# Kernel optimization log

Hardware: AMD Instinct MI355X
Metric: run time of the kernel (lower is better)

## Reference

```python
import jax, jax.numpy as jnp
import numpy as np

N_ZONE, E_ZONE = 100000, 2000000
N_OUT, E_OUT = 50000, 1000000
N_GND, E_GND = 50000, 1000000
HID = 64


def _gcn_conv(x, W, b, edge_index, edge_weight, num_nodes):
    """PyG GCNConv with normalize=True, add_self_loops=True (fill_value=1).
    out[i] = sum_{e: col[e]=i} d^-1/2[row]*w_e*d^-1/2[col] * (xW)[row[e]]
             + d^-1[i]*(xW)[i] + b
    """
    row, col = edge_index[0], edge_index[1]
    ew = edge_weight.reshape(-1)  # [E,1] -> [E]
    # degree includes self-loop weight of 1
    deg = jax.ops.segment_sum(ew, col, num_segments=num_nodes) + 1.0
    dinv = jnp.where(deg > 0, jax.lax.rsqrt(deg), 0.0)
    norm = dinv[row] * ew * dinv[col]  # [E]
    h = x @ W  # [N, HID] transform first (tiny in-dim)
    agg = jax.ops.segment_sum(norm[:, None] * h[row], col, num_segments=num_nodes)
    agg = agg + (dinv * dinv)[:, None] * h  # self-loop term
    return agg + b


def setup_inputs() -> dict:
    key = jax.random.key(0)
    ks = jax.random.split(key, 16)
    inp = {}
    inp["x_zone"] = jax.random.normal(ks[0], (N_ZONE, 2), dtype=jnp.float32)
    inp["x_outdoor"] = jax.random.normal(ks[1], (N_OUT, 3), dtype=jnp.float32)
    inp["x_ground"] = jax.random.normal(ks[2], (N_GND, 1), dtype=jnp.float32)
    inp["edge_index_zone"] = jax.random.randint(ks[3], (2, E_ZONE), 0, N_ZONE, dtype=jnp.int32)
    inp["edge_index_outdoor"] = jax.random.randint(ks[4], (2, E_OUT), 0, N_OUT, dtype=jnp.int32)
    inp["edge_index_ground"] = jax.random.randint(ks[5], (2, E_GND), 0, N_GND, dtype=jnp.int32)
    # learned params: GCN weights/biases + per-edge attribute parameters
    inp["W_zone"] = jax.random.normal(ks[6], (2, HID), dtype=jnp.float32) * 0.5
    inp["W_outdoor"] = jax.random.normal(ks[7], (3, HID), dtype=jnp.float32) * 0.5
    inp["W_ground"] = jax.random.normal(ks[8], (1, HID), dtype=jnp.float32) * 0.5
    inp["b_zone"] = jnp.zeros((HID,), dtype=jnp.float32)
    inp["b_outdoor"] = jnp.zeros((HID,), dtype=jnp.float32)
    inp["b_ground"] = jnp.zeros((HID,), dtype=jnp.float32)
    # positive edge weights so symmetric normalization deg^-1/2 is finite
    inp["edge_attr_zone"] = jax.random.uniform(ks[9], (E_ZONE, 1), dtype=jnp.float32, minval=0.1, maxval=1.0)
    inp["edge_attr_outdoor"] = jax.random.uniform(ks[10], (E_OUT, 1), dtype=jnp.float32, minval=0.1, maxval=1.0)
    inp["edge_attr_ground"] = jax.random.uniform(ks[11], (E_GND, 1), dtype=jnp.float32, minval=0.1, maxval=1.0)
    return inp


def reference(x_zone, x_outdoor, x_ground,
              edge_index_zone, edge_index_outdoor, edge_index_ground,
              W_zone, W_outdoor, W_ground,
              b_zone, b_outdoor, b_ground,
              edge_attr_zone, edge_attr_outdoor, edge_attr_ground):
    z = _gcn_conv(x_zone, W_zone, b_zone, edge_index_zone, edge_attr_zone, N_ZONE)
    o = _gcn_conv(x_outdoor, W_outdoor, b_outdoor, edge_index_outdoor, edge_attr_outdoor, N_OUT)
    g = _gcn_conv(x_ground, W_ground, b_ground, edge_index_ground, edge_attr_ground, N_GND)
    return (jax.nn.relu(z), jax.nn.relu(o), jax.nn.relu(g))
```

## Files before the change

kernel.cpp:

```cpp
#include <hip/hip_runtime.h>

#define N_ZONE 100000
#define E_ZONE 2000000
#define N_OUT  50000
#define E_OUT  1000000
#define N_GND  50000
#define E_GND  1000000
#define HID    64
#define N_TOT   (N_ZONE + N_OUT + N_GND)
#define E_TOTAL (E_ZONE + E_OUT + E_GND)

#define RANGE   2048
#define RSHIFT  11
#define NBZ     49
#define NBO     25
#define NBG     25
#define NBUCKET (NBZ + NBO + NBG)
#define SL      16
#define CAP     49152
#define OUT_PAD_BASE (NBZ * RANGE)
#define GND_PAD_BASE ((NBZ + NBO) * RANGE)
#define PAD_TOT      (NBUCKET * RANGE)

#define CHUNK  4096
#define NCHUNK ((E_TOTAL + CHUNK - 1) / CHUNK)

#define KUF 8

#define WCUR  0
#define WREC  128
#define WPDEG (WREC + 2 * NBUCKET * CAP)
#define WPSZ  (WPDEG + NBUCKET * SL * RANGE)
#define WPSO  (WPSZ + NBZ * SL * RANGE * 2)
#define WPSG  (WPSO + NBO * SL * RANGE * 3)
#define WDINV (WPSG + NBG * SL * RANGE)
#define WYZ   (WDINV + PAD_TOT)
#define WYO   (WYZ + 2 * N_ZONE)
#define WYG   (WYO + 4 * N_OUT)
#define WUZ   (WYG + N_GND)
#define WUO   (WUZ + 2 * N_ZONE)
#define WUG   (WUO + 4 * N_OUT)
#define WTOT  (WUG + N_GND)
#define FAST_WS_BYTES ((size_t)WTOT * 4)

__global__ void k_bin(const int* __restrict__ eiz, const float* __restrict__ wz,
                      const int* __restrict__ eio, const float* __restrict__ wo,
                      const int* __restrict__ eig, const float* __restrict__ wg,
                      unsigned* __restrict__ cur, uint2* __restrict__ rec) {
    __shared__ unsigned la[CHUNK];
    __shared__ float    lw[CHUNK];
    __shared__ unsigned char lbk[CHUNK];
    __shared__ unsigned hist[NBUCKET];
    __shared__ unsigned sbase[NBUCKET + 1];
    __shared__ unsigned gbase[NBUCKET];
    int tid = threadIdx.x;
    for (int b = tid; b < NBUCKET; b += 256) hist[b] = 0;
    __syncthreads();
    int t0 = blockIdx.x * CHUNK;
    unsigned mya[CHUNK / 256], mybk[CHUNK / 256], myr[CHUNK / 256];
    float myw[CHUNK / 256];
#pragma unroll
    for (int i = 0; i < CHUNK / 256; i++) {
        int t = t0 + i * 256 + tid;
        unsigned b = 0xFFFFFFFFu;
        if (t < E_TOTAL) {
            int row, col; float w;
            if (t < E_ZONE) { row = eiz[t]; col = eiz[E_ZONE + t]; w = wz[t]; b = col >> RSHIFT; }
            else if (t < E_ZONE + E_OUT) { int e = t - E_ZONE; row = eio[e]; col = eio[E_OUT + e]; w = wo[e]; b = NBZ + (col >> RSHIFT); }
            else { int e = t - E_ZONE - E_OUT; row = eig[e]; col = eig[E_GND + e]; w = wg[e]; b = NBZ + NBO + (col >> RSHIFT); }
            mya[i] = ((unsigned)(col & (RANGE - 1)) << 17) | (unsigned)row;
            myw[i] = w;
            myr[i] = atomicAdd(&hist[b], 1u);
        }
        mybk[i] = b;
    }
    __syncthreads();
    if (tid == 0) {
        unsigned acc = 0;
        for (int b = 0; b < NBUCKET; b++) { sbase[b] = acc; acc += hist[b]; }
        sbase[NBUCKET] = acc;
    }
    __syncthreads();
    if (tid < NBUCKET)
        gbase[tid] = hist[tid] ? atomicAdd(&cur[tid], hist[tid]) : 0u;
#pragma unroll
    for (int i = 0; i < CHUNK / 256; i++) {
        if (mybk[i] < NBUCKET) {
            unsigned p = sbase[mybk[i]] + myr[i];
            la[p] = mya[i]; lw[p] = myw[i];
            lbk[p] = (unsigned char)mybk[i];
        }
    }
    __syncthreads();
    unsigned total = sbase[NBUCKET];
    unsigned p = tid;
    for (; p + 768u < total; p += 1024u) {
#pragma unroll
        for (int u = 0; u < 4; u++) {
            unsigned pp = p + 256u * u;
            unsigned b = lbk[pp];
            unsigned idx = b * CAP + gbase[b] + (pp - sbase[b]);
            rec[idx] = make_uint2(la[pp], __float_as_uint(lw[pp]));
        }
    }
    for (; p < total; p += 256u) {
        unsigned b = lbk[p];
        unsigned idx = b * CAP + gbase[b] + (p - sbase[b]);
        rec[idx] = make_uint2(la[p], __float_as_uint(lw[p]));
    }
}

__global__ void k_degp(const uint2* __restrict__ rec, const unsigned* __restrict__ cur,
                       float* __restrict__ pdeg) {
    __shared__ float deg[RANGE];
    int r = blockIdx.x / SL, sl = blockIdx.x % SL, tid = threadIdx.x;
    for (int i = tid; i < RANGE; i += 256) deg[i] = 0.0f;
    __syncthreads();
    unsigned c = cur[r];
    size_t b0 = (size_t)r * CAP;
    unsigned per = (c + SL - 1) / SL;
    unsigned s0 = sl * per, s1 = s0 + per; if (s1 > c) s1 = c;
    unsigned j = s0 + tid;
    for (; j + 256u * (KUF - 1) < s1; j += 256u * KUF) {
        uint2 q[KUF];
#pragma unroll
        for (int u = 0; u < KUF; u++) q[u] = rec[b0 + j + 256u * u];
#pragma unroll
        for (int u = 0; u < KUF; u++)
            atomicAdd(&deg[(q[u].x >> 17) & (RANGE - 1)], __uint_as_float(q[u].y));
    }
    if (j < s1) {
        uint2 q[KUF];
#pragma unroll
        for (int u = 0; u < KUF; u++) {
            unsigned jj = j + 256u * u;
            q[u] = rec[b0 + (jj < s1 ? jj : j)];
        }
#pragma unroll
        for (int u = 0; u < KUF; u++)
            if (j + 256u * u < s1)
                atomicAdd(&deg[(q[u].x >> 17) & (RANGE - 1)], __uint_as_float(q[u].y));
    }
    __syncthreads();
    float* o = pdeg + (size_t)blockIdx.x * RANGE;
    for (int i = tid * 4; i < RANGE; i += 1024)
        *(float4*)&o[i] = *(float4*)&deg[i];
}

__global__ void k_dinvy(const float* __restrict__ xz, const float* __restrict__ xo,
                        const float* __restrict__ xg, float* __restrict__ ws) {
    int p = blockIdx.x * blockDim.x + threadIdx.x;
    if (p >= PAD_TOT) return;
    int r = p >> RSHIFT, i = p & (RANGE - 1);
    float d = 1.0f;
#pragma unroll
    for (int sl = 0; sl < SL; sl++)
        d += ws[WPDEG + (size_t)(r * SL + sl) * RANGE + i];
    float di = rsqrtf(d);
    ws[WDINV + p] = di;
    if (p < OUT_PAD_BASE) {
        if (p < N_ZONE) {
            ws[WYZ + 2 * p]     = di * xz[2 * p];
            ws[WYZ + 2 * p + 1] = di * xz[2 * p + 1];
        }
    } else if (p < GND_PAD_BASE) {
        int idx = p - OUT_PAD_BASE;
        if (idx < N_OUT) {
            ws[WYO + 4 * idx]     = di * xo[3 * idx];
            ws[WYO + 4 * idx + 1] = di * xo[3 * idx + 1];
            ws[WYO + 4 * idx + 2] = di * xo[3 * idx + 2];
            ws[WYO + 4 * idx + 3] = 0.0f;
        }
    } else {
        int idx = p - GND_PAD_BASE;
        if (idx < N_GND) ws[WYG + idx] = di * xg[idx];
    }
}

__global__ void k_sp(float* __restrict__ ws) {
    __shared__ __align__(16) float s[RANGE * 3];
    int r = blockIdx.x / SL, sl = blockIdx.x % SL, tid = threadIdx.x;
    const unsigned* cur = (const unsigned*)(ws + WCUR);
    const uint2* rec = (const uint2*)(ws + WREC);
    int ch, rg; size_t yoff, psoff;
    if (r < NBZ)            { ch = 2; rg = r;             yoff = WYZ; psoff = WPSZ; }
    else if (r < NBZ + NBO) { ch = 3; rg = r - NBZ;       yoff = WYO; psoff = WPSO; }
    else                    { ch = 1; rg = r - NBZ - NBO; yoff = WYG; psoff = WPSG; }
    int tot = RANGE * ch;
    for (int i = tid; i < tot; i += 256) s[i] = 0.0f;
    __syncthreads();
    unsigned c = cur[r];
    size_t b0 = (size_t)r * CAP;
    unsigned per = (c + SL - 1) / SL;
    unsigned s0 = sl * per, s1 = s0 + per; if (s1 > c) s1 = c;
    if (ch == 2) {
        const float2* y = (const float2*)(ws + yoff);
        unsigned j = s0 + tid;
        for (; j + 256u * (KUF - 1) < s1; j += 256u * KUF) {
            uint2 q[KUF];
#pragma unroll
            for (int u = 0; u < KUF; u++) q[u] = rec[b0 + j + 256u * u];
            float2 yv[KUF];
#pragma unroll
            for (int u = 0; u < KUF; u++) yv[u] = y[q[u].x & 0x1FFFFu];
#pragma unroll
            for (int u = 0; u < KUF; u++) {
                unsigned colr = (q[u].x >> 17) & (RANGE - 1);
                float w = __uint_as_float(q[u].y);
                atomicAdd(&s[colr * 2],     w * yv[u].x);
                atomicAdd(&s[colr * 2 + 1], w * yv[u].y);
            }
        }
        if (j < s1) {
            uint2 q[KUF];
#pragma unroll
            for (int u = 0; u < KUF; u++) {
                unsigned jj = j + 256u * u;
                q[u] = rec[b0 + (jj < s1 ? jj : j)];
            }
            float2 yv[KUF];
#pragma unroll
            for (int u = 0; u < KUF; u++) yv[u] = y[q[u].x & 0x1FFFFu];
#pragma unroll
            for (int u = 0; u < KUF; u++)
                if (j + 256u * u < s1) {
                    unsigned colr = (q[u].x >> 17) & (RANGE - 1);
                    float w = __uint_as_float(q[u].y);
                    atomicAdd(&s[colr * 2],     w * yv[u].x);
                    atomicAdd(&s[colr * 2 + 1], w * yv[u].y);
                }
        }
    } else if (ch == 3) {
        const float4* y = (const float4*)(ws + yoff);
        unsigned j = s0 + tid;
        for (; j + 256u * (KUF - 1) < s1; j += 256u * KUF) {
            uint2 q[KUF];
#pragma unroll
            for (int u = 0; u < KUF; u++) q[u] = rec[b0 + j + 256u * u];
            float4 yv[KUF];
#pragma unroll
            for (int u = 0; u < KUF; u++) yv[u] = y[q[u].x & 0x1FFFFu];
#pragma unroll
            for (int u = 0; u < KUF; u++) {
                unsigned colr = (q[u].x >> 17) & (RANGE - 1);
                float w = __uint_as_float(q[u].y);
                atomicAdd(&s[colr * 3],     w * yv[u].x);
                atomicAdd(&s[colr * 3 + 1], w * yv[u].y);
                atomicAdd(&s[colr * 3 + 2], w * yv[u].z);
            }
        }
        if (j < s1) {
            uint2 q[KUF];
#pragma unroll
            for (int u = 0; u < KUF; u++) {
                unsigned jj = j + 256u * u;
                q[u] = rec[b0 + (jj < s1 ? jj : j)];
            }
            float4 yv[KUF];
#pragma unroll
            for (int u = 0; u < KUF; u++) yv[u] = y[q[u].x & 0x1FFFFu];
#pragma unroll
            for (int u = 0; u < KUF; u++)
                if (j + 256u * u < s1) {
                    unsigned colr = (q[u].x >> 17) & (RANGE - 1);
                    float w = __uint_as_float(q[u].y);
                    atomicAdd(&s[colr * 3],     w * yv[u].x);
                    atomicAdd(&s[colr * 3 + 1], w * yv[u].y);
                    atomicAdd(&s[colr * 3 + 2], w * yv[u].z);
                }
        }
    } else {
        const float* y = ws + yoff;
        unsigned j = s0 + tid;
        for (; j + 256u * (KUF - 1) < s1; j += 256u * KUF) {
            uint2 q[KUF];
#pragma unroll
            for (int u = 0; u < KUF; u++) q[u] = rec[b0 + j + 256u * u];
            float yv[KUF];
#pragma unroll
            for (int u = 0; u < KUF; u++) yv[u] = y[q[u].x & 0x1FFFFu];
#pragma unroll
            for (int u = 0; u < KUF; u++)
                atomicAdd(&s[(q[u].x >> 17) & (RANGE - 1)], __uint_as_float(q[u].y) * yv[u]);
        }
        if (j < s1) {
            uint2 q[KUF];
#pragma unroll
            for (int u = 0; u < KUF; u++) {
                unsigned jj = j + 256u * u;
                q[u] = rec[b0 + (jj < s1 ? jj : j)];
            }
            float yv[KUF];
#pragma unroll
            for (int u = 0; u < KUF; u++) yv[u] = y[q[u].x & 0x1FFFFu];
#pragma unroll
            for (int u = 0; u < KUF; u++)
                if (j + 256u * u < s1)
                    atomicAdd(&s[(q[u].x >> 17) & (RANGE - 1)], __uint_as_float(q[u].y) * yv[u]);
        }
    }
    __syncthreads();
    float* o = ws + psoff + (size_t)(rg * SL + sl) * tot;
    for (int i = tid * 4; i < tot; i += 1024)
        *(float4*)&o[i] = *(float4*)&s[i];
}

__global__ void k_u(float* __restrict__ ws) {
    int p = blockIdx.x * blockDim.x + threadIdx.x;
    if (p >= PAD_TOT) return;
    int r = p >> RSHIFT, i = p & (RANGE - 1);
    float di = ws[WDINV + p];
    if (p < OUT_PAD_BASE) {
        if (p >= N_ZONE) return;
        float s0 = ws[WYZ + 2 * p], s1 = ws[WYZ + 2 * p + 1];
#pragma unroll
        for (int sl = 0; sl < SL; sl++) {
            const float* ps = ws + WPSZ + (size_t)(r * SL + sl) * RANGE * 2;
            s0 += ps[2 * i]; s1 += ps[2 * i + 1];
        }
        ws[WUZ + 2 * p] = di * s0; ws[WUZ + 2 * p + 1] = di * s1;
    } else if (p < GND_PAD_BASE) {
        int idx = p - OUT_PAD_BASE;
        if (idx >= N_OUT) return;
        int rg = r - NBZ;
        float s0 = ws[WYO + 4 * idx], s1 = ws[WYO + 4 * idx + 1], s2 = ws[WYO + 4 * idx + 2];
#pragma unroll
        for (int sl = 0; sl < SL; sl++) {
            const float* ps = ws + WPSO + (size_t)(rg * SL + sl) * RANGE * 3;
            s0 += ps[3 * i]; s1 += ps[3 * i + 1]; s2 += ps[3 * i + 2];
        }
        ws[WUO + 4 * idx] = di * s0; ws[WUO + 4 * idx + 1] = di * s1; ws[WUO + 4 * idx + 2] = di * s2;
    } else {
        int idx = p - GND_PAD_BASE;
        if (idx >= N_GND) return;
        int rg = r - NBZ - NBO;
        float s0 = ws[WYG + idx];
#pragma unroll
        for (int sl = 0; sl < SL; sl++)
            s0 += ws[WPSG + (size_t)(rg * SL + sl) * RANGE + i];
        ws[WUG + idx] = di * s0;
    }
}

__global__ void k_fin2(const float* __restrict__ ws,
                       const float* __restrict__ Wz, const float* __restrict__ bz,
                       const float* __restrict__ Wo, const float* __restrict__ bo,
                       const float* __restrict__ Wg, const float* __restrict__ bg,
                       float* __restrict__ out) {
    int t = blockIdx.x * blockDim.x + threadIdx.x;
    const int TZ4 = N_ZONE * 16, TO4 = TZ4 + N_OUT * 16, TG4 = TO4 + N_GND * 16;
    if (t < TZ4) {
        int i = t >> 4, jb = (t & 15) << 2;
        float u0 = ws[WUZ + 2 * i], u1 = ws[WUZ + 2 * i + 1];
        float4 w0 = *(const float4*)(Wz + jb);
        float4 w1 = *(const float4*)(Wz + HID + jb);
        float4 bv = *(const float4*)(bz + jb);
        float4 o;
        o.x = fmaxf(bv.x + u0 * w0.x + u1 * w1.x, 0.0f);
        o.y = fmaxf(bv.y + u0 * w0.y + u1 * w1.y, 0.0f);
        o.z = fmaxf(bv.z + u0 * w0.z + u1 * w1.z, 0.0f);
        o.w = fmaxf(bv.w + u0 * w0.w + u1 * w1.w, 0.0f);
        *(float4*)(out + i * HID + jb) = o;
    } else if (t < TO4) {
        int q = t - TZ4;
        int i = q >> 4, jb = (q & 15) << 2;
        const float* u = ws + WUO + 4 * i;
        float u0 = u[0], u1 = u[1], u2 = u[2];
        float4 w0 = *(const float4*)(Wo + jb);
        float4 w1 = *(const float4*)(Wo + HID + jb);
        float4 w2 = *(const float4*)(Wo + 2 * HID + jb);
        float4 bv = *(const float4*)(bo + jb);
        float4 o;
        o.x = fmaxf(bv.x + u0 * w0.x + u1 * w1.x + u2 * w2.x, 0.0f);
        o.y = fmaxf(bv.y + u0 * w0.y + u1 * w1.y + u2 * w2.y, 0.0f);
        o.z = fmaxf(bv.z + u0 * w0.z + u1 * w1.z + u2 * w2.z, 0.0f);
        o.w = fmaxf(bv.w + u0 * w0.w + u1 * w1.w + u2 * w2.w, 0.0f);
        *(float4*)(out + N_ZONE * HID + i * HID + jb) = o;
    } else if (t < TG4) {
        int q = t - TO4;
        int i = q >> 4, jb = (q & 15) << 2;
        float u0 = ws[WUG + i];
        float4 w0 = *(const float4*)(Wg + jb);
        float4 bv = *(const float4*)(bg + jb);
        float4 o;
        o.x = fmaxf(bv.x + u0 * w0.x, 0.0f);
        o.y = fmaxf(bv.y + u0 * w0.y, 0.0f);
        o.z = fmaxf(bv.z + u0 * w0.z, 0.0f);
        o.w = fmaxf(bv.w + u0 * w0.w, 0.0f);
        *(float4*)(out + (N_ZONE + N_OUT) * HID + i * HID + jb) = o;
    }
}

#define F_DEG_Z   0
#define F_DEG_O   (N_ZONE)
#define F_DEG_G   (N_ZONE + N_OUT)
#define F_DEG_TOT N_TOT
#define F_S_Z     F_DEG_TOT
#define F_S_O     (F_S_Z + N_ZONE * 2)
#define F_S_G     (F_S_O + N_OUT * 3)
#define F_TOT     (F_S_G + N_GND * 1)

__global__ void f_init(float* __restrict__ ws) {
    int i = blockIdx.x * blockDim.x + threadIdx.x;
    if (i < F_TOT) ws[i] = (i < F_DEG_TOT) ? 1.0f : 0.0f;
}
__global__ void f_deg(const int* __restrict__ eiz, const float* __restrict__ wz,
                      const int* __restrict__ eio, const float* __restrict__ wo,
                      const int* __restrict__ eig, const float* __restrict__ wg,
                      float* __restrict__ ws) {
    int t = blockIdx.x * blockDim.x + threadIdx.x;
    if (t < E_ZONE) atomicAdd(ws + F_DEG_Z + eiz[E_ZONE + t], wz[t]);
    else if (t < E_ZONE + E_OUT) { int e = t - E_ZONE; atomicAdd(ws + F_DEG_O + eio[E_OUT + e], wo[e]); }
    else if (t < E_ZONE + E_OUT + E_GND) { int e = t - E_ZONE - E_OUT; atomicAdd(ws + F_DEG_G + eig[E_GND + e], wg[e]); }
}
__global__ void f_dinv(float* __restrict__ ws) {
    int i = blockIdx.x * blockDim.x + threadIdx.x;
    if (i < F_DEG_TOT) ws[i] = 1.0f / sqrtf(ws[i]);
}
__global__ void f_scatter(const int* __restrict__ eiz, const float* __restrict__ wz, const float* __restrict__ xz,
                          const int* __restrict__ eio, const float* __restrict__ wo, const float* __restrict__ xo,
                          const int* __restrict__ eig, const float* __restrict__ wg, const float* __restrict__ xg,
                          float* __restrict__ ws) {
    int t = blockIdx.x * blockDim.x + threadIdx.x;
    if (t < E_ZONE) {
        int row = eiz[t], col = eiz[E_ZONE + t];
        float n = ws[F_DEG_Z + row] * wz[t] * ws[F_DEG_Z + col];
        atomicAdd(ws + F_S_Z + col * 2 + 0, n * xz[row * 2 + 0]);
        atomicAdd(ws + F_S_Z + col * 2 + 1, n * xz[row * 2 + 1]);
    } else if (t < E_ZONE + E_OUT) {
        int e = t - E_ZONE;
        int row = eio[e], col = eio[E_OUT + e];
        float n = ws[F_DEG_O + row] * wo[e] * ws[F_DEG_O + col];
        atomicAdd(ws + F_S_O + col * 3 + 0, n * xo[row * 3 + 0]);
        atomicAdd(ws + F_S_O + col * 3 + 1, n * xo[row * 3 + 1]);
        atomicAdd(ws + F_S_O + col * 3 + 2, n * xo[row * 3 + 2]);
    } else if (t < E_ZONE + E_OUT + E_GND) {
        int e = t - E_ZONE - E_OUT;
        int row = eig[e], col = eig[E_GND + e];
        float n = ws[F_DEG_G + row] * wg[e] * ws[F_DEG_G + col];
        atomicAdd(ws + F_S_G + col, n * xg[row]);
    }
}
__global__ void f_final(const float* __restrict__ ws,
                        const float* __restrict__ xz, const float* __restrict__ Wz, const float* __restrict__ bz,
                        const float* __restrict__ xo, const float* __restrict__ Wo, const float* __restrict__ bo,
                        const float* __restrict__ xg, const float* __restrict__ Wg, const float* __restrict__ bg,
                        float* __restrict__ out) {
    int t = blockIdx.x * blockDim.x + threadIdx.x;
    const int TZ = N_ZONE * HID, TO = TZ + N_OUT * HID, TG = TO + N_GND * HID;
    if (t < TZ) {
        int i = t >> 6, j = t & 63;
        float di = ws[F_DEG_Z + i], d2 = di * di;
        float t0 = ws[F_S_Z + i * 2 + 0] + d2 * xz[i * 2 + 0];
        float t1 = ws[F_S_Z + i * 2 + 1] + d2 * xz[i * 2 + 1];
        out[t] = fmaxf(bz[j] + t0 * Wz[j] + t1 * Wz[HID + j], 0.0f);
    } else if (t < TO) {
        int u = t - TZ;
        int i = u >> 6, j = u & 63;
        float di = ws[F_DEG_O + i], d2 = di * di;
        float t0 = ws[F_S_O + i * 3 + 0] + d2 * xo[i * 3 + 0];
        float t1 = ws[F_S_O + i * 3 + 1] + d2 * xo[i * 3 + 1];
        float t2 = ws[F_S_O + i * 3 + 2] + d2 * xo[i * 3 + 2];
        out[t] = fmaxf(bo[j] + t0 * Wo[j] + t1 * Wo[HID + j] + t2 * Wo[2 * HID + j], 0.0f);
    } else if (t < TG) {
        int u = t - TO;
        int i = u >> 6, j = u & 63;
        float di = ws[F_DEG_G + i], d2 = di * di;
        float t0 = ws[F_S_G + i] + d2 * xg[i];
        out[t] = fmaxf(bg[j] + t0 * Wg[j], 0.0f);
    }
}

extern "C" void kernel_launch(void* const* d_in, const int* in_sizes, int n_in,
                              void* d_out, int out_size, void* d_ws, size_t ws_size,
                              hipStream_t stream) {
    const float* xz = (const float*)d_in[0];
    const float* xo = (const float*)d_in[1];
    const float* xg = (const float*)d_in[2];
    const int*  eiz = (const int*)d_in[3];
    const int*  eio = (const int*)d_in[4];
    const int*  eig = (const int*)d_in[5];
    const float* Wz = (const float*)d_in[6];
    const float* Wo = (const float*)d_in[7];
    const float* Wg = (const float*)d_in[8];
    const float* bz = (const float*)d_in[9];
    const float* bo = (const float*)d_in[10];
    const float* bg = (const float*)d_in[11];
    const float* wz = (const float*)d_in[12];
    const float* wo = (const float*)d_in[13];
    const float* wg = (const float*)d_in[14];
    float* out = (float*)d_out;
    float* ws  = (float*)d_ws;

    const int B = 256;

    if (ws_size >= FAST_WS_BYTES) {
        unsigned* cur = (unsigned*)(ws + WCUR);
        uint2* rec = (uint2*)(ws + WREC);
        hipMemsetAsync(cur, 0, 128 * 4, stream);
        k_bin<<<NCHUNK, B, 0, stream>>>(eiz, wz, eio, wo, eig, wg, cur, rec);
        k_degp<<<NBUCKET * SL, B, 0, stream>>>(rec, cur, ws + WPDEG);
        k_dinvy<<<(PAD_TOT + B - 1) / B, B, 0, stream>>>(xz, xo, xg, ws);
        k_sp<<<NBUCKET * SL, B, 0, stream>>>(ws);
        k_u<<<(PAD_TOT + B - 1) / B, B, 0, stream>>>(ws);
        k_fin2<<<(N_TOT * HID / 4 + B - 1) / B, B, 0, stream>>>(ws, Wz, bz, Wo, bo, Wg, bg, out);
    } else {
        const int E_TOT = E_TOTAL, OUT_TOT = N_TOT * HID;
        f_init<<<(F_TOT + B - 1) / B, B, 0, stream>>>(ws);
        f_deg<<<(E_TOT + B - 1) / B, B, 0, stream>>>(eiz, wz, eio, wo, eig, wg, ws);
        f_dinv<<<(F_DEG_TOT + B - 1) / B, B, 0, stream>>>(ws);
        f_scatter<<<(E_TOT + B - 1) / B, B, 0, stream>>>(eiz, wz, xz, eio, wo, xo, eig, wg, xg, ws);
        f_final<<<(OUT_TOT + B - 1) / B, B, 0, stream>>>(ws, xz, Wz, bz, xo, Wo, bo, xg, Wg, bg, out);
    }
}
```

Before: 246.7 us.

## Compute degrees with global atomics from raw edges and load y via relaxed atomic loads

Replaces the per-bucket shared-memory degree kernel, which read the binned records, with a kernel that reads the destination indices and edge weights straight from the inputs as int4/float4 and atomically adds into a zeroed degree array in global memory. This drops the 16-way partial-degree reduction in k_dinvy and the second pass over the records. The gather of y in k_sp now uses relaxed agent-scope atomic loads, split into two 8-byte loads for the 3-channel case, apparently to change caching behaviour. The cost is 4M global float atomics with contention and a possibly less efficient gather.

```diff
diff --git a/kernel.cpp b/kernel.cpp
--- a/kernel.cpp
+++ b/kernel.cpp
@@ -42,6 +42,15 @@
 #define WUG   (WUO + 4 * N_OUT)
 #define WTOT  (WUG + N_GND)
 #define FAST_WS_BYTES ((size_t)WTOT * 4)
+
+__device__ __forceinline__ float ld_bypass_f32(const float* p) {
+    return __hip_atomic_load(p, __ATOMIC_RELAXED, __HIP_MEMORY_SCOPE_AGENT);
+}
+__device__ __forceinline__ float2 ld_bypass_f2(const float* p) {
+    unsigned long long v = __hip_atomic_load((const unsigned long long*)p,
+                                             __ATOMIC_RELAXED, __HIP_MEMORY_SCOPE_AGENT);
+    float2 r; __builtin_memcpy(&r, &v, 8); return r;
+}
 
 __global__ void k_bin(const int* __restrict__ eiz, const float* __restrict__ wz,
                       const int* __restrict__ eio, const float* __restrict__ wo,
@@ -110,52 +119,39 @@
     }
 }
 
-__global__ void k_degp(const uint2* __restrict__ rec, const unsigned* __restrict__ cur,
-                       float* __restrict__ pdeg) {
-    __shared__ float deg[RANGE];
-    int r = blockIdx.x / SL, sl = blockIdx.x % SL, tid = threadIdx.x;
-    for (int i = tid; i < RANGE; i += 256) deg[i] = 0.0f;
-    __syncthreads();
-    unsigned c = cur[r];
-    size_t b0 = (size_t)r * CAP;
-    unsigned per = (c + SL - 1) / SL;
-    unsigned s0 = sl * per, s1 = s0 + per; if (s1 > c) s1 = c;
-    unsigned j = s0 + tid;
-    for (; j + 256u * (KUF - 1) < s1; j += 256u * KUF) {
-        uint2 q[KUF];
-#pragma unroll
-        for (int u = 0; u < KUF; u++) q[u] = rec[b0 + j + 256u * u];
-#pragma unroll
-        for (int u = 0; u < KUF; u++)
-            atomicAdd(&deg[(q[u].x >> 17) & (RANGE - 1)], __uint_as_float(q[u].y));
-    }
-    if (j < s1) {
-        uint2 q[KUF];
-#pragma unroll
-        for (int u = 0; u < KUF; u++) {
-            unsigned jj = j + 256u * u;
-            q[u] = rec[b0 + (jj < s1 ? jj : j)];
-        }
-#pragma unroll
-        for (int u = 0; u < KUF; u++)
-            if (j + 256u * u < s1)
-                atomicAdd(&deg[(q[u].x >> 17) & (RANGE - 1)], __uint_as_float(q[u].y));
-    }
-    __syncthreads();
-    float* o = pdeg + (size_t)blockIdx.x * RANGE;
-    for (int i = tid * 4; i < RANGE; i += 1024)
-        *(float4*)&o[i] = *(float4*)&deg[i];
+__global__ void k_dega(const int* __restrict__ eiz, const float* __restrict__ wz,
+                       const int* __restrict__ eio, const float* __restrict__ wo,
+                       const int* __restrict__ eig, const float* __restrict__ wg,
+                       float* __restrict__ deg) {
+    int g = blockIdx.x * blockDim.x + threadIdx.x;
+    const int GZ = E_ZONE / 4, GO = GZ + E_OUT / 4, GG = GO + E_GND / 4;
+    int4 c4; float4 w4; int base;
+    if (g < GZ) {
+        c4 = ((const int4*)(eiz + E_ZONE))[g];
+        w4 = ((const float4*)wz)[g];
+        base = 0;
+    } else if (g < GO) {
+        int e = g - GZ;
+        c4 = ((const int4*)(eio + E_OUT))[e];
+        w4 = ((const float4*)wo)[e];
+        base = OUT_PAD_BASE;
+    } else if (g < GG) {
+        int e = g - GO;
+        c4 = ((const int4*)(eig + E_GND))[e];
+        w4 = ((const float4*)wg)[e];
+        base = GND_PAD_BASE;
+    } else return;
+    atomicAdd(deg + base + c4.x, w4.x);
+    atomicAdd(deg + base + c4.y, w4.y);
+    atomicAdd(deg + base + c4.z, w4.z);
+    atomicAdd(deg + base + c4.w, w4.w);
 }
 
 __global__ void k_dinvy(const float* __restrict__ xz, const float* __restrict__ xo,
                         const float* __restrict__ xg, float* __restrict__ ws) {
     int p = blockIdx.x * blockDim.x + threadIdx.x;
     if (p >= PAD_TOT) return;
-    int r = p >> RSHIFT, i = p & (RANGE - 1);
-    float d = 1.0f;
-#pragma unroll
-    for (int sl = 0; sl < SL; sl++)
-        d += ws[WPDEG + (size_t)(r * SL + sl) * RANGE + i];
+    float d = 1.0f + ws[WPDEG + p];
     float di = rsqrtf(d);
     ws[WDINV + p] = di;
     if (p < OUT_PAD_BASE) {
@@ -194,7 +190,7 @@
     unsigned per = (c + SL - 1) / SL;
     unsigned s0 = sl * per, s1 = s0 + per; if (s1 > c) s1 = c;
     if (ch == 2) {
-        const float2* y = (const float2*)(ws + yoff);
+        const float* y = ws + yoff;
         unsigned j = s0 + tid;
         for (; j + 256u * (KUF - 1) < s1; j += 256u * KUF) {
             uint2 q[KUF];
@@ -202,7 +198,7 @@
             for (int u = 0; u < KUF; u++) q[u] = rec[b0 + j + 256u * u];
             float2 yv[KUF];
 #pragma unroll
-            for (int u = 0; u < KUF; u++) yv[u] = y[q[u].x & 0x1FFFFu];
+            for (int u = 0; u < KUF; u++) yv[u] = ld_bypass_f2(y + 2 * (q[u].x & 0x1FFFFu));
 #pragma unroll
             for (int u = 0; u < KUF; u++) {
                 unsigned colr = (q[u].x >> 17) & (RANGE - 1);
@@ -220,7 +216,7 @@
             }
             float2 yv[KUF];
 #pragma unroll
-            for (int u = 0; u < KUF; u++) yv[u] = y[q[u].x & 0x1FFFFu];
+            for (int u = 0; u < KUF; u++) yv[u] = ld_bypass_f2(y + 2 * (q[u].x & 0x1FFFFu));
 #pragma unroll
             for (int u = 0; u < KUF; u++)
                 if (j + 256u * u < s1) {
@@ -231,22 +227,26 @@
                 }
         }
     } else if (ch == 3) {
-        const float4* y = (const float4*)(ws + yoff);
+        const float* y = ws + yoff;
         unsigned j = s0 + tid;
         for (; j + 256u * (KUF - 1) < s1; j += 256u * KUF) {
             uint2 q[KUF];
 #pragma unroll
             for (int u = 0; u < KUF; u++) q[u] = rec[b0 + j + 256u * u];
-            float4 yv[KUF];
-#pragma unroll
-            for (int u = 0; u < KUF; u++) yv[u] = y[q[u].x & 0x1FFFFu];
+            float2 ylo[KUF], yhi[KUF];
+#pragma unroll
+            for (int u = 0; u < KUF; u++) {
+                unsigned row = q[u].x & 0x1FFFFu;
+                ylo[u] = ld_bypass_f2(y + 4 * row);
+                yhi[u] = ld_bypass_f2(y + 4 * row + 2);
+            }
 #pragma unroll
             for (int u = 0; u < KUF; u++) {
                 unsigned colr = (q[u].x >> 17) & (RANGE - 1);
                 float w = __uint_as_float(q[u].y);
-                atomicAdd(&s[colr * 3],     w * yv[u].x);
-                atomicAdd(&s[colr * 3 + 1], w * yv[u].y);
-                atomicAdd(&s[colr * 3 + 2], w * yv[u].z);
+                atomicAdd(&s[colr * 3],     w * ylo[u].x);
+                atomicAdd(&s[colr * 3 + 1], w * ylo[u].y);
+                atomicAdd(&s[colr * 3 + 2], w * yhi[u].x);
             }
         }
         if (j < s1) {
@@ -256,17 +256,21 @@
                 unsigned jj = j + 256u * u;
                 q[u] = rec[b0 + (jj < s1 ? jj : j)];
             }
-            float4 yv[KUF];
-#pragma unroll
-            for (int u = 0; u < KUF; u++) yv[u] = y[q[u].x & 0x1FFFFu];
+            float2 ylo[KUF], yhi[KUF];
+#pragma unroll
+            for (int u = 0; u < KUF; u++) {
+                unsigned row = q[u].x & 0x1FFFFu;
+                ylo[u] = ld_bypass_f2(y + 4 * row);
+                yhi[u] = ld_bypass_f2(y + 4 * row + 2);
+            }
 #pragma unroll
             for (int u = 0; u < KUF; u++)
                 if (j + 256u * u < s1) {
                     unsigned colr = (q[u].x >> 17) & (RANGE - 1);
                     float w = __uint_as_float(q[u].y);
-                    atomicAdd(&s[colr * 3],     w * yv[u].x);
-                    atomicAdd(&s[colr * 3 + 1], w * yv[u].y);
-                    atomicAdd(&s[colr * 3 + 2], w * yv[u].z);
+                    atomicAdd(&s[colr * 3],     w * ylo[u].x);
+                    atomicAdd(&s[colr * 3 + 1], w * ylo[u].y);
+                    atomicAdd(&s[colr * 3 + 2], w * yhi[u].x);
                 }
         }
     } else {
@@ -278,7 +282,7 @@
             for (int u = 0; u < KUF; u++) q[u] = rec[b0 + j + 256u * u];
             float yv[KUF];
 #pragma unroll
-            for (int u = 0; u < KUF; u++) yv[u] = y[q[u].x & 0x1FFFFu];
+            for (int u = 0; u < KUF; u++) yv[u] = ld_bypass_f32(y + (q[u].x & 0x1FFFFu));
 #pragma unroll
             for (int u = 0; u < KUF; u++)
                 atomicAdd(&s[(q[u].x >> 17) & (RANGE - 1)], __uint_as_float(q[u].y) * yv[u]);
@@ -292,7 +296,7 @@
             }
             float yv[KUF];
 #pragma unroll
-            for (int u = 0; u < KUF; u++) yv[u] = y[q[u].x & 0x1FFFFu];
+            for (int u = 0; u < KUF; u++) yv[u] = ld_bypass_f32(y + (q[u].x & 0x1FFFFu));
 #pragma unroll
             for (int u = 0; u < KUF; u++)
                 if (j + 256u * u < s1)
@@ -498,8 +502,9 @@
         unsigned* cur = (unsigned*)(ws + WCUR);
         uint2* rec = (uint2*)(ws + WREC);
         hipMemsetAsync(cur, 0, 128 * 4, stream);
+        hipMemsetAsync(ws + WPDEG, 0, (size_t)PAD_TOT * 4, stream);
+        k_dega<<<(E_TOTAL / 4 + B - 1) / B, B, 0, stream>>>(eiz, wz, eio, wo, eig, wg, ws + WPDEG);
         k_bin<<<NCHUNK, B, 0, stream>>>(eiz, wz, eio, wo, eig, wg, cur, rec);
-        k_degp<<<NBUCKET * SL, B, 0, stream>>>(rec, cur, ws + WPDEG);
         k_dinvy<<<(PAD_TOT + B - 1) / B, B, 0, stream>>>(xz, xo, xg, ws);
         k_sp<<<NBUCKET * SL, B, 0, stream>>>(ws);
         k_u<<<(PAD_TOT + B - 1) / B, B, 0, stream>>>(ws);
```

Result: slower. 423.9 us (+71.8%).
